# Performance work log

Hardware: AMD Instinct MI355X
Metric: run time of the kernel (lower is better)

The kernel has to match this reference:

```python
import jax, jax.numpy as jnp
import numpy as np

D = 768
H = 8
HD = D // H  # 96
DFF = 2048
EPS = 1e-5


def layernorm(x, g, b):
    mu = jnp.mean(x, axis=-1, keepdims=True)
    var = jnp.var(x, axis=-1, keepdims=True)
    return (x - mu) * jax.lax.rsqrt(var + EPS) * g + b


def setup_inputs() -> dict:
    key = jax.random.key(0)
    ks = jax.random.split(key, 12)
    B, L = 4, 1024
    s = lambda fan: 1.0 / np.sqrt(fan)
    return {
        "x": jax.random.normal(ks[0], (B, L, D), jnp.float32),
        "attn_bias": jax.random.normal(ks[1], (B, L, L), jnp.float32),
        "in_proj_w": jax.random.normal(ks[2], (3 * D, D), jnp.float32) * s(D),
        "in_proj_b": jnp.zeros((3 * D,), jnp.float32),
        "out_w": jax.random.normal(ks[3], (D, D), jnp.float32) * s(D),
        "out_b": jnp.zeros((D,), jnp.float32),
        "ff1_w": jax.random.normal(ks[4], (DFF, D), jnp.float32) * s(D),
        "ff1_b": jnp.zeros((DFF,), jnp.float32),
        "ff2_w": jax.random.normal(ks[5], (D, DFF), jnp.float32) * s(DFF),
        "ff2_b": jnp.zeros((D,), jnp.float32),
        "ln1_g": jnp.ones((D,), jnp.float32),
        "ln1_b": jnp.zeros((D,), jnp.float32),
        "ln2_g": jnp.ones((D,), jnp.float32),
        "ln2_b": jnp.zeros((D,), jnp.float32),
    }


def reference(x, attn_bias, in_proj_w, in_proj_b, out_w, out_b,
              ff1_w, ff1_b, ff2_w, ff2_b, ln1_g, ln1_b, ln2_g, ln2_b):
    B, L, _ = x.shape
    # combined QKV projection (torch nn.MultiheadAttention in_proj)
    qkv = x @ in_proj_w.T + in_proj_b  # [B,L,3D]
    q, k, v = jnp.split(qkv, 3, axis=-1)
    q = q.reshape(B, L, H, HD).transpose(0, 2, 1, 3)  # [B,H,L,hd]
    k = k.reshape(B, L, H, HD).transpose(0, 2, 1, 3)
    v = v.reshape(B, L, H, HD).transpose(0, 2, 1, 3)
    scale = 1.0 / np.sqrt(HD)
    scores = jnp.einsum('bhld,bhmd->bhlm', q, k) * scale + attn_bias[:, None, :, :]
    probs = jax.nn.softmax(scores, axis=-1)
    attn = jnp.einsum('bhlm,bhmd->bhld', probs, v)  # [B,H,L,hd]
    attn = attn.transpose(0, 2, 1, 3).reshape(B, L, D)
    attn = attn @ out_w.T + out_b
    x = layernorm(x + attn, ln1_g, ln1_b)
    h = jax.nn.gelu(x @ ff1_w.T + ff1_b, approximate=False) @ ff2_w.T + ff2_b
    x = layernorm(x + h, ln2_g, ln2_b)
    return x
```

## Files before the change

kernel.cpp:

```cpp
#include <hip/hip_runtime.h>

typedef __bf16 bf16x8 __attribute__((ext_vector_type(8)));
typedef float f32x4 __attribute__((ext_vector_type(4)));
typedef unsigned short u16x8 __attribute__((ext_vector_type(8)));
typedef short s16x4 __attribute__((ext_vector_type(4)));

__device__ __forceinline__ unsigned short f2b(float f) {
    union { float f; unsigned u; } v; v.f = f;
    unsigned r = (v.u + 0x7fffu + ((v.u >> 16) & 1u)) >> 16;
    return (unsigned short)r;
}

__device__ __forceinline__ void load_lds16(const void* g, void* l) {
    __builtin_amdgcn_global_load_lds(
        (const __attribute__((address_space(1))) unsigned int*)g,
        (__attribute__((address_space(3))) unsigned int*)l,
        16, 0, 0);
}

__global__ void cvt_kernel(const float* __restrict__ in, unsigned short* __restrict__ out, int n4) {
    int i = blockIdx.x * 256 + threadIdx.x;
    if (i < n4) {
        f32x4 v = ((const f32x4*)in)[i];
        s16x4 o;
        o.x = (short)f2b(v.x);
        o.y = (short)f2b(v.y);
        o.z = (short)f2b(v.z);
        o.w = (short)f2b(v.w);
        ((s16x4*)out)[i] = o;
    }
}

template <int BM, int BN, int EPI>
__global__ __launch_bounds__(512, 2)
void gemm_pipe(const unsigned short* __restrict__ A, const unsigned short* __restrict__ Bm,
               const float* __restrict__ bias, void* __restrict__ Cout,
               int M, int N, int K) {
    constexpr int ACH = BM / 8;
    constexpr int TC  = (BM + BN) / 8;
    constexpr int CPW = TC / 8;
    constexpr int MR = 4;
    constexpr int NR = BN / 64;
    __shared__ unsigned short As[3][BM * 64];
    __shared__ unsigned short Bs[3][BN * 64];
    const int tid = threadIdx.x, lane = tid & 63, wid = tid >> 6;
    const int l15 = lane & 15, lq = lane >> 4;
    const int wr = wid >> 2, wc = wid & 3;

    const int nwg = gridDim.x * gridDim.y;
    int bid = blockIdx.y * gridDim.x + blockIdx.x;
    bid = (bid & 7) * (nwg >> 3) + (bid >> 3);
    const int bx = bid % gridDim.x, by = bid / gridDim.x;
    const int m0 = by * BM, n0 = bx * BN;

    const int srow = lane >> 3;
    const int scol = ((lane & 7) ^ srow) * 8;

    f32x4 acc[MR][NR];
#pragma unroll
    for (int i = 0; i < MR; i++)
#pragma unroll
        for (int j = 0; j < NR; j++) acc[i][j] = 0.0f;

    auto stage = [&](int buf, int kt) {
        const int kb = kt * 64;
#pragma unroll
        for (int i = 0; i < CPW; ++i) {
            const int c = wid * CPW + i;
            if (c < ACH) {
                load_lds16(A + (size_t)(m0 + c * 8 + srow) * K + kb + scol,
                           (char*)As[buf] + c * 1024);
            } else {
                load_lds16(Bm + (size_t)(n0 + (c - ACH) * 8 + srow) * K + kb + scol,
                           (char*)Bs[buf] + (c - ACH) * 1024);
            }
        }
    };

    auto compute = [&](int buf) {
#pragma unroll
        for (int kc = 0; kc < 2; ++kc) {
            const int cb = kc * 64;
            const int sw = (l15 & 7) << 4;
            bf16x8 af[MR], bf[NR];
#pragma unroll
            for (int mi = 0; mi < MR; mi++) {
                const int row = wr * 64 + mi * 16 + l15;
                af[mi] = *(const bf16x8*)((const char*)As[buf] + row * 128 + ((cb + lq * 16) ^ sw));
            }
#pragma unroll
            for (int ni = 0; ni < NR; ni++) {
                const int row = wc * (BN / 4) + ni * 16 + l15;
                bf[ni] = *(const bf16x8*)((const char*)Bs[buf] + row * 128 + ((cb + lq * 16) ^ sw));
            }
#pragma unroll
            for (int mi = 0; mi < MR; mi++)
#pragma unroll
                for (int ni = 0; ni < NR; ni++)
                    acc[mi][ni] = __builtin_amdgcn_mfma_f32_16x16x32_bf16(af[mi], bf[ni], acc[mi][ni], 0, 0, 0);
        }
    };

    const int nkt = K / 64;
    stage(0, 0);
    stage(1, 1);
    stage(2, 2);
    int cur = 0;
    for (int t = 0; t < nkt; ++t) {
        if (t <= nkt - 3)      asm volatile("s_waitcnt vmcnt(12)" ::: "memory");
        else if (t == nkt - 2) asm volatile("s_waitcnt vmcnt(6)" ::: "memory");
        else                   asm volatile("s_waitcnt vmcnt(0)" ::: "memory");
        __builtin_amdgcn_s_barrier();
        asm volatile("" ::: "memory");
        compute(cur);
        asm volatile("" ::: "memory");
        __builtin_amdgcn_s_barrier();
        if (t + 3 < nkt) stage(cur, t + 3);
        cur = (cur == 2) ? 0 : cur + 1;
    }

#pragma unroll
    for (int mi = 0; mi < MR; mi++) {
#pragma unroll
        for (int ni = 0; ni < NR; ni++) {
            const int col = n0 + wc * (BN / 4) + ni * 16 + l15;
            const float bv = bias[col];
#pragma unroll
            for (int r = 0; r < 4; r++) {
                const int row = m0 + wr * 64 + mi * 16 + lq * 4 + r;
                float v = acc[mi][ni][r] + bv;
                if constexpr (EPI == 2) {
                    v = 0.5f * v * (1.0f + erff(v * 0.7071067811865475f));
                }
                if constexpr (EPI == 1) {
                    ((float*)Cout)[(size_t)row * N + col] = v;
                } else {
                    ((unsigned short*)Cout)[(size_t)row * N + col] = f2b(v);
                }
            }
        }
    }
}

__global__ __launch_bounds__(256, 2)
void attn_kernel(const unsigned short* __restrict__ qkv,
                 const float* __restrict__ bias,
                 unsigned short* __restrict__ out) {
    const int L = 1024, TD = 2304, HD = 96;
    const int qt = blockIdx.x, h = blockIdx.y, b = blockIdx.z;
    const int tid = threadIdx.x, lane = tid & 63, wid = tid >> 6;
    const int l15 = lane & 15, lq = lane >> 4;
    const int q0 = qt * 64;
    const float scale = 0.10206207261596576f;

    __shared__ unsigned short Ks[64][104];
    __shared__ unsigned short Vt[96][72];
    __shared__ unsigned short Ps[4][16][72];

    bf16x8 qf[3];
    const int qrow = q0 + wid * 16 + l15;
#pragma unroll
    for (int kc = 0; kc < 3; kc++)
        qf[kc] = *(const bf16x8*)(qkv + (size_t)(b * L + qrow) * TD + h * HD + kc * 32 + lq * 8);

    f32x4 o[6];
#pragma unroll
    for (int df = 0; df < 6; df++) o[df] = 0.0f;
    float mrow[4] = {-1e30f, -1e30f, -1e30f, -1e30f};
    float lrow[4] = {0.f, 0.f, 0.f, 0.f};

    for (int kv0 = 0; kv0 < L; kv0 += 64) {
#pragma unroll
        for (int i = 0; i < 3; i++) {
            int c = i * 256 + tid;
            int row = c / 12, cc = c % 12;
            *(f32x4*)&Ks[row][cc * 8] =
                *(const f32x4*)(qkv + (size_t)(b * L + kv0 + row) * TD + 768 + h * HD + cc * 8);
        }
#pragma unroll
        for (int i = 0; i < 3; i++) {
            int dblk = i * 4 + wid;
            int m = lane;
            u16x8 v = *(const u16x8*)(qkv + (size_t)(b * L + kv0 + m) * TD + 1536 + h * HD + dblk * 8);
#pragma unroll
            for (int j = 0; j < 8; j++) Vt[dblk * 8 + j][m] = v[j];
        }
        __syncthreads();

        f32x4 s[4];
#pragma unroll
        for (int nf = 0; nf < 4; nf++) s[nf] = 0.0f;
#pragma unroll
        for (int kc = 0; kc < 3; kc++) {
#pragma unroll
            for (int nf = 0; nf < 4; nf++) {
                bf16x8 kf = *(const bf16x8*)&Ks[nf * 16 + l15][kc * 32 + lq * 8];
                s[nf] = __builtin_amdgcn_mfma_f32_16x16x32_bf16(qf[kc], kf, s[nf], 0, 0, 0);
            }
        }
#pragma unroll
        for (int nf = 0; nf < 4; nf++) {
            int colg = kv0 + nf * 16 + l15;
#pragma unroll
            for (int r = 0; r < 4; r++) {
                int rowg = q0 + wid * 16 + lq * 4 + r;
                s[nf][r] = s[nf][r] * scale + bias[((size_t)b * L + rowg) * L + colg];
            }
        }
        float pm[4];
#pragma unroll
        for (int r = 0; r < 4; r++) {
            float mx = fmaxf(fmaxf(s[0][r], s[1][r]), fmaxf(s[2][r], s[3][r]));
#pragma unroll
            for (int d = 1; d < 16; d <<= 1) mx = fmaxf(mx, __shfl_xor(mx, d, 64));
            pm[r] = mx;
        }
        float alpha[4];
#pragma unroll
        for (int r = 0; r < 4; r++) {
            float mn = fmaxf(mrow[r], pm[r]);
            alpha[r] = __expf(mrow[r] - mn);
            mrow[r] = mn;
        }
        float rs[4] = {0.f, 0.f, 0.f, 0.f};
#pragma unroll
        for (int nf = 0; nf < 4; nf++)
#pragma unroll
            for (int r = 0; r < 4; r++) {
                float p = __expf(s[nf][r] - mrow[r]);
                s[nf][r] = p;
                rs[r] += p;
            }
#pragma unroll
        for (int r = 0; r < 4; r++) {
#pragma unroll
            for (int d = 1; d < 16; d <<= 1) rs[r] += __shfl_xor(rs[r], d, 64);
            lrow[r] = lrow[r] * alpha[r] + rs[r];
        }
#pragma unroll
        for (int nf = 0; nf < 4; nf++)
#pragma unroll
            for (int r = 0; r < 4; r++)
                Ps[wid][lq * 4 + r][nf * 16 + l15] = f2b(s[nf][r]);
#pragma unroll
        for (int df = 0; df < 6; df++)
#pragma unroll
            for (int r = 0; r < 4; r++) o[df][r] *= alpha[r];
        asm volatile("s_waitcnt lgkmcnt(0)" ::: "memory");
#pragma unroll
        for (int kc = 0; kc < 2; kc++) {
            bf16x8 pf = *(const bf16x8*)&Ps[wid][l15][kc * 32 + lq * 8];
#pragma unroll
            for (int df = 0; df < 6; df++) {
                bf16x8 vf = *(const bf16x8*)&Vt[df * 16 + l15][kc * 32 + lq * 8];
                o[df] = __builtin_amdgcn_mfma_f32_16x16x32_bf16(pf, vf, o[df], 0, 0, 0);
            }
        }
        __syncthreads();
    }
#pragma unroll
    for (int r = 0; r < 4; r++) {
        float inv = 1.0f / lrow[r];
        int rowg = q0 + wid * 16 + lq * 4 + r;
#pragma unroll
        for (int df = 0; df < 6; df++)
            out[((size_t)b * L + rowg) * 768 + h * 96 + df * 16 + l15] = f2b(o[df][r] * inv);
    }
}

template <int WRITE_B>
__global__ __launch_bounds__(256, 4)
void ln_kernel(const float* __restrict__ x, const float* __restrict__ res,
               const float* __restrict__ g, const float* __restrict__ bvec,
               float* __restrict__ outf, unsigned short* __restrict__ outb) {
    const int Dm = 768;
    int row = blockIdx.x;
    const float* xr = x + (size_t)row * Dm;
    const float* rr = res + (size_t)row * Dm;
    int tid = threadIdx.x;
    float v[3];
    float sum = 0.f, sq = 0.f;
#pragma unroll
    for (int j = 0; j < 3; j++) {
        int i = tid + j * 256;
        float t = xr[i] + rr[i];
        v[j] = t;
        sum += t;
        sq += t * t;
    }
#pragma unroll
    for (int d = 1; d < 64; d <<= 1) {
        sum += __shfl_xor(sum, d, 64);
        sq += __shfl_xor(sq, d, 64);
    }
    __shared__ float ps[8];
    int lane = tid & 63, wid = tid >> 6;
    if (lane == 0) { ps[wid] = sum; ps[wid + 4] = sq; }
    __syncthreads();
    sum = ps[0] + ps[1] + ps[2] + ps[3];
    sq = ps[4] + ps[5] + ps[6] + ps[7];
    float mu = sum * (1.0f / 768.0f);
    float var = sq * (1.0f / 768.0f) - mu * mu;
    float rsg = rsqrtf(var + 1e-5f);
#pragma unroll
    for (int j = 0; j < 3; j++) {
        int i = tid + j * 256;
        float o = (v[j] - mu) * rsg * g[i] + bvec[i];
        outf[(size_t)row * Dm + i] = o;
        if constexpr (WRITE_B) outb[(size_t)row * Dm + i] = f2b(o);
    }
}

extern "C" void kernel_launch(void* const* d_in, const int* in_sizes, int n_in,
                              void* d_out, int out_size, void* d_ws, size_t ws_size,
                              hipStream_t stream) {
    (void)in_sizes; (void)n_in; (void)out_size; (void)ws_size;
    const float* x         = (const float*)d_in[0];
    const float* attn_bias = (const float*)d_in[1];
    const float* in_proj_w = (const float*)d_in[2];
    const float* in_proj_b = (const float*)d_in[3];
    const float* out_w     = (const float*)d_in[4];
    const float* out_b     = (const float*)d_in[5];
    const float* ff1_w     = (const float*)d_in[6];
    const float* ff1_b     = (const float*)d_in[7];
    const float* ff2_w     = (const float*)d_in[8];
    const float* ff2_b     = (const float*)d_in[9];
    const float* ln1_g     = (const float*)d_in[10];
    const float* ln1_b     = (const float*)d_in[11];
    const float* ln2_g     = (const float*)d_in[12];
    const float* ln2_b     = (const float*)d_in[13];

    const int NTOK = 4096;
    char* ws = (char*)d_ws;
    size_t off = 0;
    auto alloc = [&](size_t bytes) { void* p = ws + off; off += (bytes + 255) & ~(size_t)255; return p; };
    unsigned short* xb    = (unsigned short*)alloc((size_t)NTOK * 768 * 2);
    unsigned short* wqkv  = (unsigned short*)alloc((size_t)2304 * 768 * 2);
    unsigned short* wout  = (unsigned short*)alloc((size_t)768 * 768 * 2);
    unsigned short* wff1  = (unsigned short*)alloc((size_t)2048 * 768 * 2);
    unsigned short* wff2  = (unsigned short*)alloc((size_t)768 * 2048 * 2);
    unsigned short* qkvb  = (unsigned short*)alloc((size_t)NTOK * 2304 * 2);
    unsigned short* attnb = (unsigned short*)alloc((size_t)NTOK * 768 * 2);
    float*          aproj = (float*)alloc((size_t)NTOK * 768 * 4);
    float*          x1f   = (float*)alloc((size_t)NTOK * 768 * 4);
    unsigned short* x1b   = (unsigned short*)alloc((size_t)NTOK * 768 * 2);
    unsigned short* h1b  = qkvb;
    float*          ff2o = aproj;

    cvt_kernel<<<dim3((NTOK * 768 / 4) / 256), 256, 0, stream>>>(x, xb, NTOK * 768 / 4);
    cvt_kernel<<<dim3((2304 * 768 / 4) / 256), 256, 0, stream>>>(in_proj_w, wqkv, 2304 * 768 / 4);
    cvt_kernel<<<dim3((768 * 768 / 4) / 256), 256, 0, stream>>>(out_w, wout, 768 * 768 / 4);
    cvt_kernel<<<dim3((2048 * 768 / 4) / 256), 256, 0, stream>>>(ff1_w, wff1, 2048 * 768 / 4);
    cvt_kernel<<<dim3((768 * 2048 / 4) / 256), 256, 0, stream>>>(ff2_w, wff2, 768 * 2048 / 4);

    gemm_pipe<128, 256, 0><<<dim3(2304 / 256, NTOK / 128), 512, 0, stream>>>(xb, wqkv, in_proj_b, qkvb, NTOK, 2304, 768);
    attn_kernel<<<dim3(16, 8, 4), 256, 0, stream>>>(qkvb, attn_bias, attnb);
    gemm_pipe<128, 128, 1><<<dim3(768 / 128, NTOK / 128), 512, 0, stream>>>(attnb, wout, out_b, aproj, NTOK, 768, 768);
    ln_kernel<1><<<dim3(NTOK), 256, 0, stream>>>(x, aproj, ln1_g, ln1_b, x1f, x1b);
    gemm_pipe<128, 256, 2><<<dim3(2048 / 256, NTOK / 128), 512, 0, stream>>>(x1b, wff1, ff1_b, h1b, NTOK, 2048, 768);
    gemm_pipe<128, 128, 1><<<dim3(768 / 128, NTOK / 128), 512, 0, stream>>>(h1b, wff2, ff2_b, ff2o, NTOK, 768, 2048);
    ln_kernel<0><<<dim3(NTOK), 256, 0, stream>>>(x1f, ff2o, ln2_g, ln2_b, (float*)d_out, nullptr);
}
```

Measured before the change: 178.6 us.

## Stage GEMM and attention epilogues through LDS for vectorized stores; vectorize layernorm

The GEMM epilogue now writes accumulators into a per-wave swizzled LDS tile that reuses the pipeline buffers, then each lane emits 16-byte coalesced global stores instead of scattered scalar stores. The attention output goes through a small LDS tile the same way before its bf16 stores. The layernorm kernel switches to float4 loads and stores with 192 active threads. The GEMM launch bounds drop to one block per SM, which frees registers but may lower occupancy, and the epilogues add LDS traffic.

After: 180.7 us. Within noise of the previous version (+1.2%).

```diff
diff --git a/kernel.cpp b/kernel.cpp
--- a/kernel.cpp
+++ b/kernel.cpp
@@ -32,7 +32,7 @@
 }
 
 template <int BM, int BN, int EPI>
-__global__ __launch_bounds__(512, 2)
+__global__ __launch_bounds__(512, 1)
 void gemm_pipe(const unsigned short* __restrict__ A, const unsigned short* __restrict__ Bm,
                const float* __restrict__ bias, void* __restrict__ Cout,
                int M, int N, int K) {
@@ -41,8 +41,14 @@
     constexpr int CPW = TC / 8;
     constexpr int MR = 4;
     constexpr int NR = BN / 64;
-    __shared__ unsigned short As[3][BM * 64];
-    __shared__ unsigned short Bs[3][BN * 64];
+    constexpr int WN = BN / 4;
+    constexpr int WSTR = (WN == 64) ? 72 : 36;
+    constexpr int ABYTES = BM * 128;
+    constexpr int BBYTES = BN * 128;
+    constexpr int SMEM_BYTES = 3 * (ABYTES + BBYTES);
+    static_assert(8 * 64 * WSTR * 4 <= SMEM_BYTES, "epilogue fits");
+    __shared__ char smem[SMEM_BYTES];
+
     const int tid = threadIdx.x, lane = tid & 63, wid = tid >> 6;
     const int l15 = lane & 15, lq = lane >> 4;
     const int wr = wid >> 2, wc = wid & 3;
@@ -69,10 +75,10 @@
             const int c = wid * CPW + i;
             if (c < ACH) {
                 load_lds16(A + (size_t)(m0 + c * 8 + srow) * K + kb + scol,
-                           (char*)As[buf] + c * 1024);
+                           smem + buf * ABYTES + c * 1024);
             } else {
                 load_lds16(Bm + (size_t)(n0 + (c - ACH) * 8 + srow) * K + kb + scol,
-                           (char*)Bs[buf] + (c - ACH) * 1024);
+                           smem + 3 * ABYTES + buf * BBYTES + (c - ACH) * 1024);
             }
         }
     };
@@ -86,12 +92,12 @@
 #pragma unroll
             for (int mi = 0; mi < MR; mi++) {
                 const int row = wr * 64 + mi * 16 + l15;
-                af[mi] = *(const bf16x8*)((const char*)As[buf] + row * 128 + ((cb + lq * 16) ^ sw));
+                af[mi] = *(const bf16x8*)(smem + buf * ABYTES + row * 128 + ((cb + lq * 16) ^ sw));
             }
 #pragma unroll
             for (int ni = 0; ni < NR; ni++) {
-                const int row = wc * (BN / 4) + ni * 16 + l15;
-                bf[ni] = *(const bf16x8*)((const char*)Bs[buf] + row * 128 + ((cb + lq * 16) ^ sw));
+                const int row = wc * WN + ni * 16 + l15;
+                bf[ni] = *(const bf16x8*)(smem + 3 * ABYTES + buf * BBYTES + row * 128 + ((cb + lq * 16) ^ sw));
             }
 #pragma unroll
             for (int mi = 0; mi < MR; mi++)
@@ -119,24 +125,64 @@
         cur = (cur == 2) ? 0 : cur + 1;
     }
 
+    float* ew = (float*)(smem + wid * 64 * WSTR * 4);
 #pragma unroll
     for (int mi = 0; mi < MR; mi++) {
 #pragma unroll
         for (int ni = 0; ni < NR; ni++) {
-            const int col = n0 + wc * (BN / 4) + ni * 16 + l15;
-            const float bv = bias[col];
+            const int cl = ni * 16 + l15;
+            const float bv = bias[n0 + wc * WN + cl];
 #pragma unroll
             for (int r = 0; r < 4; r++) {
-                const int row = m0 + wr * 64 + mi * 16 + lq * 4 + r;
+                const int rl = mi * 16 + lq * 4 + r;
                 float v = acc[mi][ni][r] + bv;
                 if constexpr (EPI == 2) {
                     v = 0.5f * v * (1.0f + erff(v * 0.7071067811865475f));
                 }
-                if constexpr (EPI == 1) {
-                    ((float*)Cout)[(size_t)row * N + col] = v;
-                } else {
-                    ((unsigned short*)Cout)[(size_t)row * N + col] = f2b(v);
-                }
+                ew[rl * WSTR + (cl ^ (lq << 3))] = v;
+            }
+        }
+    }
+    asm volatile("s_waitcnt lgkmcnt(0)" ::: "memory");
+
+    if constexpr (WN == 64) {
+        const int r8 = lane >> 3, c8 = lane & 7;
+#pragma unroll
+        for (int j = 0; j < 8; j++) {
+            const int row = r8 + 8 * j;
+            const int po = c8 ^ ((row >> 2) & 3);
+            f32x4 a = *(const f32x4*)(ew + row * WSTR + po * 8);
+            f32x4 b = *(const f32x4*)(ew + row * WSTR + po * 8 + 4);
+            const int grow = m0 + wr * 64 + row;
+            const int gcol = n0 + wc * WN + c8 * 8;
+            if constexpr (EPI == 1) {
+                *(f32x4*)&((float*)Cout)[(size_t)grow * N + gcol] = a;
+                *(f32x4*)&((float*)Cout)[(size_t)grow * N + gcol + 4] = b;
+            } else {
+                u16x8 p;
+#pragma unroll
+                for (int e = 0; e < 4; e++) { p[e] = f2b(a[e]); p[e + 4] = f2b(b[e]); }
+                *(u16x8*)&((unsigned short*)Cout)[(size_t)grow * N + gcol] = p;
+            }
+        }
+    } else {
+        const int r8 = lane >> 2, c8 = lane & 3;
+#pragma unroll
+        for (int j = 0; j < 4; j++) {
+            const int row = r8 + 16 * j;
+            const int po = c8 ^ ((row >> 2) & 3);
+            f32x4 a = *(const f32x4*)(ew + row * WSTR + po * 8);
+            f32x4 b = *(const f32x4*)(ew + row * WSTR + po * 8 + 4);
+            const int grow = m0 + wr * 64 + row;
+            const int gcol = n0 + wc * WN + c8 * 8;
+            if constexpr (EPI == 1) {
+                *(f32x4*)&((float*)Cout)[(size_t)grow * N + gcol] = a;
+                *(f32x4*)&((float*)Cout)[(size_t)grow * N + gcol + 4] = b;
+            } else {
+                u16x8 p;
+#pragma unroll
+                for (int e = 0; e < 4; e++) { p[e] = f2b(a[e]); p[e + 4] = f2b(b[e]); }
+                *(u16x8*)&((unsigned short*)Cout)[(size_t)grow * N + gcol] = p;
             }
         }
     }
@@ -156,6 +202,7 @@
     __shared__ unsigned short Ks[64][104];
     __shared__ unsigned short Vt[96][72];
     __shared__ unsigned short Ps[4][16][72];
+    __shared__ float Ot[4][16][100];
 
     bf16x8 qf[3];
     const int qrow = q0 + wid * 16 + l15;
@@ -258,13 +305,32 @@
         }
         __syncthreads();
     }
+
 #pragma unroll
     for (int r = 0; r < 4; r++) {
         float inv = 1.0f / lrow[r];
-        int rowg = q0 + wid * 16 + lq * 4 + r;
-#pragma unroll
-        for (int df = 0; df < 6; df++)
-            out[((size_t)b * L + rowg) * 768 + h * 96 + df * 16 + l15] = f2b(o[df][r] * inv);
+        const int rl = lq * 4 + r;
+#pragma unroll
+        for (int df = 0; df < 6; df++) {
+            const int cl = df * 16 + l15;
+            Ot[wid][rl][cl ^ (lq << 3)] = o[df][r] * inv;
+        }
+    }
+    asm volatile("s_waitcnt lgkmcnt(0)" ::: "memory");
+    {
+        const int r = lane >> 2, c8 = lane & 3;
+        const int rowg = q0 + wid * 16 + r;
+#pragma unroll
+        for (int it = 0; it < 3; it++) {
+            const int oc = c8 + 4 * it;
+            const int po = oc ^ ((r >> 2) & 3);
+            f32x4 a = *(const f32x4*)&Ot[wid][r][po * 8];
+            f32x4 bb = *(const f32x4*)&Ot[wid][r][po * 8 + 4];
+            u16x8 p;
+#pragma unroll
+            for (int e = 0; e < 4; e++) { p[e] = f2b(a[e]); p[e + 4] = f2b(bb[e]); }
+            *(u16x8*)&out[((size_t)b * L + rowg) * 768 + h * 96 + oc * 8] = p;
+        }
     }
 }
 
@@ -275,18 +341,15 @@
                float* __restrict__ outf, unsigned short* __restrict__ outb) {
     const int Dm = 768;
     int row = blockIdx.x;
-    const float* xr = x + (size_t)row * Dm;
-    const float* rr = res + (size_t)row * Dm;
     int tid = threadIdx.x;
-    float v[3];
+    f32x4 v = {0.f, 0.f, 0.f, 0.f};
     float sum = 0.f, sq = 0.f;
-#pragma unroll
-    for (int j = 0; j < 3; j++) {
-        int i = tid + j * 256;
-        float t = xr[i] + rr[i];
-        v[j] = t;
-        sum += t;
-        sq += t * t;
+    if (tid < 192) {
+        f32x4 xv = ((const f32x4*)(x + (size_t)row * Dm))[tid];
+        f32x4 rv = ((const f32x4*)(res + (size_t)row * Dm))[tid];
+        v = xv + rv;
+        sum = v.x + v.y + v.z + v.w;
+        sq = v.x * v.x + v.y * v.y + v.z * v.z + v.w * v.w;
     }
 #pragma unroll
     for (int d = 1; d < 64; d <<= 1) {
@@ -302,12 +365,19 @@
     float mu = sum * (1.0f / 768.0f);
     float var = sq * (1.0f / 768.0f) - mu * mu;
     float rsg = rsqrtf(var + 1e-5f);
-#pragma unroll
-    for (int j = 0; j < 3; j++) {
-        int i = tid + j * 256;
-        float o = (v[j] - mu) * rsg * g[i] + bvec[i];
-        outf[(size_t)row * Dm + i] = o;
-        if constexpr (WRITE_B) outb[(size_t)row * Dm + i] = f2b(o);
+    if (tid < 192) {
+        f32x4 gv = ((const f32x4*)g)[tid];
+        f32x4 bv = ((const f32x4*)bvec)[tid];
+        f32x4 ov;
+#pragma unroll
+        for (int e = 0; e < 4; e++) ov[e] = (v[e] - mu) * rsg * gv[e] + bv[e];
+        ((f32x4*)(outf + (size_t)row * Dm))[tid] = ov;
+        if constexpr (WRITE_B) {
+            s16x4 pb;
+#pragma unroll
+            for (int e = 0; e < 4; e++) pb[e] = (short)f2b(ov[e]);
+            ((s16x4*)(outb + (size_t)row * Dm))[tid] = pb;
+        }
     }
 }
 
```
